# Performance work log

Measured on AMD Instinct MI355X. Metric: run time of the kernel, lower is better.

Reference implementation:

```python
import jax, jax.numpy as jnp
import numpy as np
import math

N = 100000   # nodes
E = 500000   # edges
IN_C = 128
EDGE_D = 64
HEADS = 4
OUT_C = 32
HC = HEADS * OUT_C  # 128


def setup_inputs() -> dict:
    key = jax.random.key(0)
    ks = jax.random.split(key, 12)
    s_in = 1.0 / math.sqrt(IN_C)
    s_e = 1.0 / math.sqrt(EDGE_D)
    return {
        "x": jax.random.normal(ks[0], (N, IN_C), jnp.float32),
        "edge_index": jax.random.randint(ks[1], (2, E), 0, N, dtype=jnp.int32),
        "edge_attr": jax.random.normal(ks[2], (E, EDGE_D), jnp.float32),
        "Wq": jax.random.uniform(ks[3], (HC, IN_C), jnp.float32, -s_in, s_in),
        "bq": jax.random.uniform(ks[4], (HC,), jnp.float32, -s_in, s_in),
        "Wk": jax.random.uniform(ks[5], (HC, IN_C), jnp.float32, -s_in, s_in),
        "bk": jax.random.uniform(ks[6], (HC,), jnp.float32, -s_in, s_in),
        "Wv": jax.random.uniform(ks[7], (HC, IN_C), jnp.float32, -s_in, s_in),
        "bv": jax.random.uniform(ks[8], (HC,), jnp.float32, -s_in, s_in),
        "We": jax.random.uniform(ks[9], (HC, EDGE_D), jnp.float32, -s_e, s_e),
        "Ws": jax.random.uniform(ks[10], (HC, IN_C), jnp.float32, -s_in, s_in),
        "bs": jax.random.uniform(ks[11], (HC,), jnp.float32, -s_in, s_in),
    }


def reference(x, edge_index, edge_attr, Wq, bq, Wk, bk, Wv, bv, We, Ws, bs):
    src = edge_index[0]
    dst = edge_index[1]
    x_i = x[dst]                       # [E, IN_C] target-node feats
    x_j = x[src]                       # [E, IN_C] source-node feats

    e = (edge_attr @ We.T).reshape(E, HEADS, OUT_C)
    q = (x_i @ Wq.T + bq).reshape(E, HEADS, OUT_C)
    k = (x_j @ Wk.T + bk).reshape(E, HEADS, OUT_C) + e

    alpha = jnp.sum(q * k, axis=-1) / jnp.sqrt(jnp.float32(OUT_C))  # [E, H]
    # Faithful to the source: GLOBAL per-column max (not per-segment), then
    # segment-sum of exponentials over destination nodes.
    m = jnp.max(alpha, axis=0)                                      # [H]
    exp_a = jnp.exp(alpha - m)                                      # [E, H]
    denom = jax.ops.segment_sum(exp_a, dst, num_segments=N)         # [N, H]
    alpha = exp_a / (denom[dst] + 1e-16)                            # [E, H]

    v = (x_j @ Wv.T + bv).reshape(E, HEADS, OUT_C) + e
    msg = v * alpha[:, :, None]                                     # [E, H, C]

    out = jax.ops.segment_sum(msg.reshape(E, HC), dst, num_segments=N)  # [N, HC]
    out = out + (x @ Ws.T + bs)
    return out
```

## Files before the change

kernel.cpp:

```cpp
#include <hip/hip_runtime.h>
#include <hip/hip_bf16.h>
#include <math.h>

#define N_NODES 100000
#define N_EDGES 500000
#define M0 8.0f
#define INV_SQRT32 0.17677669529663687f

#define NB_HIST 1954
#define NB_PROJ 1563
#define NB_EE   3907
#define GRID_MEGA (NB_HIST + NB_PROJ + NB_EE)

typedef __attribute__((ext_vector_type(8))) short bf16x8;
typedef __attribute__((ext_vector_type(4))) float f32x4;
typedef __attribute__((ext_vector_type(8))) unsigned short us8;

static __device__ __forceinline__ unsigned short f2bf(float f) {
    __hip_bfloat16 h = __float2bfloat16(f);
    return *(unsigned short*)&h;
}

static __device__ __forceinline__ void split4(float4 v, ushort4& hv, ushort4& lv) {
    const unsigned short h0 = f2bf(v.x), h1 = f2bf(v.y),
                         h2 = f2bf(v.z), h3 = f2bf(v.w);
    hv.x = h0; hv.y = h1; hv.z = h2; hv.w = h3;
    lv.x = f2bf(v.x - __uint_as_float((unsigned)h0 << 16));
    lv.y = f2bf(v.y - __uint_as_float((unsigned)h1 << 16));
    lv.z = f2bf(v.z - __uint_as_float((unsigned)h2 << 16));
    lv.w = f2bf(v.w - __uint_as_float((unsigned)h3 << 16));
}

__global__ __launch_bounds__(256) void prep_kernel(
    const float* __restrict__ Wq, const float* __restrict__ Wk,
    const float* __restrict__ Wv, const float* __restrict__ Ws,
    const float* __restrict__ We,
    unsigned short* __restrict__ WBh, unsigned short* __restrict__ WBl,
    unsigned short* __restrict__ WEh, unsigned short* __restrict__ WEl,
    int* __restrict__ cursor)
{
    const int i = blockIdx.x * 256 + threadIdx.x;
    if (i < N_NODES) cursor[i] = 0;
    if (i < 65536) {
        const int p = i >> 14;
        const float* W = (p == 0) ? Wq : (p == 1) ? Wk : (p == 2) ? Wv : Ws;
        const float v = W[i & 16383];
        const unsigned short h = f2bf(v);
        WBh[i] = h;
        WBl[i] = f2bf(v - __uint_as_float((unsigned)h << 16));
    } else if (i < 73728) {
        const int idx = i - 65536;
        const float v = We[idx];
        const unsigned short h = f2bf(v);
        WEh[idx] = h;
        WEl[idx] = f2bf(v - __uint_as_float((unsigned)h << 16));
    }
}

__global__ __launch_bounds__(256) void mega_kernel(
    const float* __restrict__ x, const int* __restrict__ ei,
    const float* __restrict__ ea,
    const unsigned short* __restrict__ WBh, const unsigned short* __restrict__ WBl,
    const unsigned short* __restrict__ WEh, const unsigned short* __restrict__ WEl,
    const float* __restrict__ bq, const float* __restrict__ bk,
    const float* __restrict__ bv, const float* __restrict__ bs,
    float* __restrict__ Qn, float* __restrict__ Kn, float* __restrict__ Vn,
    float* __restrict__ out, unsigned short* __restrict__ Ee,
    int* __restrict__ cursor)
{
    __shared__ __align__(16) unsigned short sAh[8192];
    __shared__ __align__(16) unsigned short sAl[8192];
    __shared__ __align__(16) unsigned short sWh[8192];
    __shared__ __align__(16) unsigned short sWl[8192];

    const int t = threadIdx.x;
    const int bid = blockIdx.x;

    if (bid < NB_HIST) {
        const int e = bid * 256 + t;
        if (e < N_EDGES) atomicAdd(&cursor[ei[N_EDGES + e]], 1);
        return;
    }

    const int lane = t & 63;
    const int fr = lane & 15;
    const int fq = lane >> 4;

    if (bid < NB_HIST + NB_PROJ) {
        const long r0 = (long)(bid - NB_HIST) * 64;
        const int wid = t >> 6;

        for (int i = t; i < 2048; i += 256) {
            const int r = i >> 5;
            const int k4 = (i & 31) * 4;
            const long row = r0 + r;
            float4 v = (row < N_NODES) ? *(const float4*)&x[row * 128 + k4]
                                       : make_float4(0.f, 0.f, 0.f, 0.f);
            ushort4 hv, lv; split4(v, hv, lv);
            const int di = r * 128 + (k4 ^ ((r & 7) << 3));
            *(ushort4*)&sAh[di] = hv;
            *(ushort4*)&sAl[di] = lv;
        }

        for (int p = 0; p < 4; ++p) {
            const float* bias = (p == 0) ? bq : (p == 1) ? bk : (p == 2) ? bv : bs;
            float* dst        = (p == 0) ? Qn : (p == 1) ? Kn : (p == 2) ? Vn : out;

            f32x4 acc[4][2];
#pragma unroll
            for (int m = 0; m < 4; ++m)
#pragma unroll
                for (int n = 0; n < 2; ++n) acc[m][n] = (f32x4){0.f, 0.f, 0.f, 0.f};

            for (int kc = 0; kc < 2; ++kc) {
                __syncthreads();
                for (int i = t; i < 1024; i += 256) {
                    const int r = i >> 3;
                    const int s = i & 7;
                    const int gi = p * 16384 + r * 128 + kc * 64 + s * 8;
                    const int di = r * 64 + ((s * 8) ^ ((r & 7) << 3));
                    *(us8*)&sWh[di] = *(const us8*)&WBh[gi];
                    *(us8*)&sWl[di] = *(const us8*)&WBl[gi];
                }
                __syncthreads();

#pragma unroll
                for (int ks = 0; ks < 2; ++ks) {
                    const int kx = kc * 64 + ks * 32 + fq * 8;
                    const int kw = ks * 32 + fq * 8;
                    bf16x8 ah[4], al[4], bh[2], bl[2];
#pragma unroll
                    for (int m = 0; m < 4; ++m) {
                        const int r = m * 16 + fr;
                        const int di = r * 128 + (kx ^ ((r & 7) << 3));
                        ah[m] = *(const bf16x8*)&sAh[di];
                        al[m] = *(const bf16x8*)&sAl[di];
                    }
#pragma unroll
                    for (int n = 0; n < 2; ++n) {
                        const int r = wid * 32 + n * 16 + fr;
                        const int di = r * 64 + (kw ^ ((r & 7) << 3));
                        bh[n] = *(const bf16x8*)&sWh[di];
                        bl[n] = *(const bf16x8*)&sWl[di];
                    }
#pragma unroll
                    for (int m = 0; m < 4; ++m)
#pragma unroll
                        for (int n = 0; n < 2; ++n) {
                            acc[m][n] = __builtin_amdgcn_mfma_f32_16x16x32_bf16(
                                ah[m], bh[n], acc[m][n], 0, 0, 0);
                            acc[m][n] = __builtin_amdgcn_mfma_f32_16x16x32_bf16(
                                ah[m], bl[n], acc[m][n], 0, 0, 0);
                            acc[m][n] = __builtin_amdgcn_mfma_f32_16x16x32_bf16(
                                al[m], bh[n], acc[m][n], 0, 0, 0);
                        }
                }
            }

            float bb[2];
#pragma unroll
            for (int n = 0; n < 2; ++n) bb[n] = bias[wid * 32 + n * 16 + fr];
#pragma unroll
            for (int m = 0; m < 4; ++m) {
                const long rowb = r0 + m * 16 + fq * 4;
#pragma unroll
                for (int j = 0; j < 4; ++j) {
                    if (rowb + j < N_NODES) {
#pragma unroll
                        for (int n = 0; n < 2; ++n)
                            dst[(rowb + j) * 128 + wid * 32 + n * 16 + fr] =
                                acc[m][n][j] + bb[n];
                    }
                }
            }
        }
    } else {
        const long e0 = (long)(bid - NB_HIST - NB_PROJ) * 128;
        const int wr = (t >> 6) >> 1;
        const int wc = (t >> 6) & 1;

        for (int i = t; i < 1024; i += 256) {
            const int r = i >> 3;
            const int s = i & 7;
            const int di = r * 64 + ((s * 8) ^ ((r & 7) << 3));
            *(us8*)&sWh[di] = *(const us8*)&WEh[r * 64 + s * 8];
            *(us8*)&sWl[di] = *(const us8*)&WEl[r * 64 + s * 8];
        }
        for (int i = t; i < 2048; i += 256) {
            const int r = i >> 4;
            const int k4 = (i & 15) * 4;
            const long e = e0 + r;
            float4 v = (e < N_EDGES) ? *(const float4*)&ea[e * 64 + k4]
                                     : make_float4(0.f, 0.f, 0.f, 0.f);
            ushort4 hv, lv; split4(v, hv, lv);
            const int di = r * 64 + (k4 ^ ((r & 7) << 3));
            *(ushort4*)&sAh[di] = hv;
            *(ushort4*)&sAl[di] = lv;
        }
        __syncthreads();

        f32x4 acc[4][4];
#pragma unroll
        for (int m = 0; m < 4; ++m)
#pragma unroll
            for (int n = 0; n < 4; ++n) acc[m][n] = (f32x4){0.f, 0.f, 0.f, 0.f};

#pragma unroll
        for (int ks = 0; ks < 2; ++ks) {
            const int kk = ks * 32 + fq * 8;
            bf16x8 ah[4], al[4], bh[4], bl[4];
#pragma unroll
            for (int m = 0; m < 4; ++m) {
                const int r = wr * 64 + m * 16 + fr;
                const int di = r * 64 + (kk ^ ((r & 7) << 3));
                ah[m] = *(const bf16x8*)&sAh[di];
                al[m] = *(const bf16x8*)&sAl[di];
            }
#pragma unroll
            for (int n = 0; n < 4; ++n) {
                const int r = wc * 64 + n * 16 + fr;
                const int di = r * 64 + (kk ^ ((r & 7) << 3));
                bh[n] = *(const bf16x8*)&sWh[di];
                bl[n] = *(const bf16x8*)&sWl[di];
            }
#pragma unroll
            for (int m = 0; m < 4; ++m)
#pragma unroll
                for (int n = 0; n < 4; ++n) {
                    acc[m][n] = __builtin_amdgcn_mfma_f32_16x16x32_bf16(
                        ah[m], bh[n], acc[m][n], 0, 0, 0);
                    acc[m][n] = __builtin_amdgcn_mfma_f32_16x16x32_bf16(
                        ah[m], bl[n], acc[m][n], 0, 0, 0);
                    acc[m][n] = __builtin_amdgcn_mfma_f32_16x16x32_bf16(
                        al[m], bh[n], acc[m][n], 0, 0, 0);
                }
        }

#pragma unroll
        for (int m = 0; m < 4; ++m) {
            const long erow = e0 + wr * 64 + m * 16 + fq * 4;
#pragma unroll
            for (int j = 0; j < 4; ++j) {
                if (erow + j < N_EDGES) {
#pragma unroll
                    for (int n = 0; n < 4; ++n)
                        Ee[(erow + j) * 128 + wc * 64 + n * 16 + fr] =
                            f2bf(acc[m][n][j]);
                }
            }
        }
    }
}

__global__ __launch_bounds__(1024) void csr_scan_kernel(
    int* __restrict__ cursor, int* __restrict__ csr_off)
{
    __shared__ int wsum[16];
    const int t = threadIdx.x;
    const int lane = t & 63;
    const int wid = t >> 6;
    const int n0 = t * 100;
    const bool active = (t < 1000);

    int tsum = 0;
    if (active) {
        for (int q = 0; q < 25; ++q) {
            const int4 d = *(const int4*)&cursor[n0 + q * 4];
            tsum += d.x + d.y + d.z + d.w;
        }
    }
    int inc = tsum;
#pragma unroll
    for (int o = 1; o < 64; o <<= 1) {
        const int v = __shfl_up(inc, o, 64);
        if (lane >= o) inc += v;
    }
    if (lane == 63) wsum[wid] = inc;
    __syncthreads();
    if (t == 0) {
        int run = 0;
#pragma unroll
        for (int w = 0; w < 16; ++w) { const int v = wsum[w]; wsum[w] = run; run += v; }
        csr_off[N_NODES] = run;
    }
    __syncthreads();
    if (active) {
        int run = wsum[wid] + inc - tsum;
        for (int q = 0; q < 25; ++q) {
            const int n = n0 + q * 4;
            const int4 d = *(const int4*)&cursor[n];
            int4 offv;
            offv.x = run; run += d.x;
            offv.y = run; run += d.y;
            offv.z = run; run += d.z;
            offv.w = run; run += d.w;
            *(int4*)&csr_off[n] = offv;
            *(int4*)&cursor[n]  = offv;
        }
    }
}

__global__ __launch_bounds__(256) void csr_fill_kernel(
    const int* __restrict__ ei, int* __restrict__ cursor,
    int* __restrict__ csr_eid, int* __restrict__ csr_src)
{
    const int e = blockIdx.x * 256 + threadIdx.x;
    if (e >= N_EDGES) return;
    const int dst = ei[N_EDGES + e];
    const int pos = atomicAdd(&cursor[dst], 1);
    csr_eid[pos] = e;
    csr_src[pos] = ei[e];
}

__global__ __launch_bounds__(256) void fused_attn_kernel(
    const int* __restrict__ csr_off, const int* __restrict__ csr_eid,
    const int* __restrict__ csr_src, const unsigned short* __restrict__ Ee,
    const float* __restrict__ Qn, const float* __restrict__ Kn,
    const float* __restrict__ Vn, float* __restrict__ out)
{
    const int lane = threadIdx.x & 63;
    const int l2 = lane * 2;
    const long n = (long)blockIdx.x * 4 + (threadIdx.x >> 6);

    const int off0 = csr_off[n];
    const int off1 = csr_off[n + 1];
    const float2 q = *(const float2*)&Qn[n * 128 + l2];

    float dsum = 0.f;
    float2 acc = make_float2(0.f, 0.f);
    for (int base = off0; base < off1; base += 64) {
        const int cnt = min(64, off1 - base);
        int eid = 0, src = 0;
        if (base + lane < off1) {
            eid = csr_eid[base + lane];
            src = csr_src[base + lane];
        }
        for (int j = 0; j < cnt; ++j) {
            const long e = __shfl(eid, j, 64);
            const long s = __shfl(src, j, 64);
            const unsigned u = *(const unsigned*)&Ee[e * 128 + l2];
            const float2 k = *(const float2*)&Kn[s * 128 + l2];
            const float ea0 = __uint_as_float(u << 16);
            const float ea1 = __uint_as_float(u & 0xffff0000u);
            float p = q.x * (k.x + ea0) + q.y * (k.y + ea1);
#pragma unroll
            for (int o = 1; o < 16; o <<= 1) p += __shfl_xor(p, o, 64);
            const float an = __expf(p * INV_SQRT32 - M0);
            dsum += an;
            const float2 v = *(const float2*)&Vn[s * 128 + l2];
            acc.x = fmaf(v.x + ea0, an, acc.x);
            acc.y = fmaf(v.y + ea1, an, acc.y);
        }
    }
    const float rd = 1.f / (dsum + 1e-16f);
    float2 o = *(const float2*)&out[n * 128 + l2];
    o.x = fmaf(acc.x, rd, o.x);
    o.y = fmaf(acc.y, rd, o.y);
    *(float2*)&out[n * 128 + l2] = o;
}

extern "C" void kernel_launch(void* const* d_in, const int* in_sizes, int n_in,
                              void* d_out, int out_size, void* d_ws, size_t ws_size,
                              hipStream_t stream)
{
    const float* x  = (const float*)d_in[0];
    const int*   ei = (const int*)d_in[1];
    const float* ea = (const float*)d_in[2];
    const float* Wq = (const float*)d_in[3];
    const float* bq = (const float*)d_in[4];
    const float* Wk = (const float*)d_in[5];
    const float* bk = (const float*)d_in[6];
    const float* Wv = (const float*)d_in[7];
    const float* bv = (const float*)d_in[8];
    const float* We = (const float*)d_in[9];
    const float* Ws = (const float*)d_in[10];
    const float* bs = (const float*)d_in[11];
    float* out = (float*)d_out;

    float* ws = (float*)d_ws;
    float* Qn = ws;
    float* Kn = ws + 12800000;
    float* Vn = ws + 25600000;
    int* csr_off = (int*)(ws + 38400000);
    int* cursor  = (int*)(ws + 38500004);
    int* csr_eid = (int*)(ws + 38600004);
    int* csr_src = (int*)(ws + 39100004);
    unsigned short* WBh = (unsigned short*)(ws + 40000000);
    unsigned short* WBl = (unsigned short*)(ws + 40050000);
    unsigned short* WEh = (unsigned short*)(ws + 40100000);
    unsigned short* WEl = (unsigned short*)(ws + 40110000);
    unsigned short* Ee = (unsigned short*)((char*)d_ws + 163200032);

    prep_kernel<<<391, 256, 0, stream>>>(Wq, Wk, Wv, Ws, We,
                                         WBh, WBl, WEh, WEl, cursor);

    mega_kernel<<<GRID_MEGA, 256, 0, stream>>>(x, ei, ea,
                                               WBh, WBl, WEh, WEl,
                                               bq, bk, bv, bs,
                                               Qn, Kn, Vn, out, Ee, cursor);

    csr_scan_kernel<<<1, 1024, 0, stream>>>(cursor, csr_off);

    csr_fill_kernel<<<NB_HIST, 256, 0, stream>>>(ei, cursor, csr_eid, csr_src);

    fused_attn_kernel<<<25000, 256, 0, stream>>>(csr_off, csr_eid, csr_src, Ee,
                                                 Qn, Kn, Vn, out);
}
```

Measured before the change: 599.6 us.

## Use 512-thread mega blocks and process four edges per wave in attention

```diff
diff --git a/kernel.cpp b/kernel.cpp
--- a/kernel.cpp
+++ b/kernel.cpp
@@ -7,7 +7,7 @@
 #define M0 8.0f
 #define INV_SQRT32 0.17677669529663687f
 
-#define NB_HIST 1954
+#define NB_HIST 977
 #define NB_PROJ 1563
 #define NB_EE   3907
 #define GRID_MEGA (NB_HIST + NB_PROJ + NB_EE)
@@ -57,7 +57,7 @@
     }
 }
 
-__global__ __launch_bounds__(256) void mega_kernel(
+__global__ __launch_bounds__(512, 4) void mega_kernel(
     const float* __restrict__ x, const int* __restrict__ ei,
     const float* __restrict__ ea,
     const unsigned short* __restrict__ WBh, const unsigned short* __restrict__ WBl,
@@ -77,20 +77,20 @@
     const int bid = blockIdx.x;
 
     if (bid < NB_HIST) {
-        const int e = bid * 256 + t;
+        const int e = bid * 512 + t;
         if (e < N_EDGES) atomicAdd(&cursor[ei[N_EDGES + e]], 1);
         return;
     }
 
     const int lane = t & 63;
+    const int wid = t >> 6;
     const int fr = lane & 15;
     const int fq = lane >> 4;
 
     if (bid < NB_HIST + NB_PROJ) {
         const long r0 = (long)(bid - NB_HIST) * 64;
-        const int wid = t >> 6;
-
-        for (int i = t; i < 2048; i += 256) {
+
+        for (int i = t; i < 2048; i += 512) {
             const int r = i >> 5;
             const int k4 = (i & 31) * 4;
             const long row = r0 + r;
@@ -106,15 +106,13 @@
             const float* bias = (p == 0) ? bq : (p == 1) ? bk : (p == 2) ? bv : bs;
             float* dst        = (p == 0) ? Qn : (p == 1) ? Kn : (p == 2) ? Vn : out;
 
-            f32x4 acc[4][2];
-#pragma unroll
-            for (int m = 0; m < 4; ++m)
-#pragma unroll
-                for (int n = 0; n < 2; ++n) acc[m][n] = (f32x4){0.f, 0.f, 0.f, 0.f};
+            f32x4 acc[4];
+#pragma unroll
+            for (int m = 0; m < 4; ++m) acc[m] = (f32x4){0.f, 0.f, 0.f, 0.f};
 
             for (int kc = 0; kc < 2; ++kc) {
                 __syncthreads();
-                for (int i = t; i < 1024; i += 256) {
+                for (int i = t; i < 1024; i += 512) {
                     const int r = i >> 3;
                     const int s = i & 7;
                     const int gi = p * 16384 + r * 128 + kc * 64 + s * 8;
@@ -128,7 +126,7 @@
                 for (int ks = 0; ks < 2; ++ks) {
                     const int kx = kc * 64 + ks * 32 + fq * 8;
                     const int kw = ks * 32 + fq * 8;
-                    bf16x8 ah[4], al[4], bh[2], bl[2];
+                    bf16x8 ah[4], al[4], bh, bl;
 #pragma unroll
                     for (int m = 0; m < 4; ++m) {
                         const int r = m * 16 + fr;
@@ -136,57 +134,48 @@
                         ah[m] = *(const bf16x8*)&sAh[di];
                         al[m] = *(const bf16x8*)&sAl[di];
                     }
-#pragma unroll
-                    for (int n = 0; n < 2; ++n) {
-                        const int r = wid * 32 + n * 16 + fr;
+                    {
+                        const int r = wid * 16 + fr;
                         const int di = r * 64 + (kw ^ ((r & 7) << 3));
-                        bh[n] = *(const bf16x8*)&sWh[di];
-                        bl[n] = *(const bf16x8*)&sWl[di];
+                        bh = *(const bf16x8*)&sWh[di];
+                        bl = *(const bf16x8*)&sWl[di];
                     }
 #pragma unroll
-                    for (int m = 0; m < 4; ++m)
-#pragma unroll
-                        for (int n = 0; n < 2; ++n) {
-                            acc[m][n] = __builtin_amdgcn_mfma_f32_16x16x32_bf16(
-                                ah[m], bh[n], acc[m][n], 0, 0, 0);
-                            acc[m][n] = __builtin_amdgcn_mfma_f32_16x16x32_bf16(
-                                ah[m], bl[n], acc[m][n], 0, 0, 0);
-                            acc[m][n] = __builtin_amdgcn_mfma_f32_16x16x32_bf16(
-                                al[m], bh[n], acc[m][n], 0, 0, 0);
-                        }
-                }
-            }
-
-            float bb[2];
-#pragma unroll
-            for (int n = 0; n < 2; ++n) bb[n] = bias[wid * 32 + n * 16 + fr];
+                    for (int m = 0; m < 4; ++m) {
+                        acc[m] = __builtin_amdgcn_mfma_f32_16x16x32_bf16(
+                            ah[m], bh, acc[m], 0, 0, 0);
+                        acc[m] = __builtin_amdgcn_mfma_f32_16x16x32_bf16(
+                            ah[m], bl, acc[m], 0, 0, 0);
+                        acc[m] = __builtin_amdgcn_mfma_f32_16x16x32_bf16(
+                            al[m], bh, acc[m], 0, 0, 0);
+                    }
+                }
+            }
+
+            const float bb = bias[wid * 16 + fr];
 #pragma unroll
             for (int m = 0; m < 4; ++m) {
                 const long rowb = r0 + m * 16 + fq * 4;
 #pragma unroll
                 for (int j = 0; j < 4; ++j) {
-                    if (rowb + j < N_NODES) {
-#pragma unroll
-                        for (int n = 0; n < 2; ++n)
-                            dst[(rowb + j) * 128 + wid * 32 + n * 16 + fr] =
-                                acc[m][n][j] + bb[n];
-                    }
+                    if (rowb + j < N_NODES)
+                        dst[(rowb + j) * 128 + wid * 16 + fr] = acc[m][j] + bb;
                 }
             }
         }
     } else {
         const long e0 = (long)(bid - NB_HIST - NB_PROJ) * 128;
-        const int wr = (t >> 6) >> 1;
-        const int wc = (t >> 6) & 1;
-
-        for (int i = t; i < 1024; i += 256) {
+        const int wr = wid >> 2;
+        const int wc = wid & 3;
+
+        for (int i = t; i < 1024; i += 512) {
             const int r = i >> 3;
             const int s = i & 7;
             const int di = r * 64 + ((s * 8) ^ ((r & 7) << 3));
             *(us8*)&sWh[di] = *(const us8*)&WEh[r * 64 + s * 8];
             *(us8*)&sWl[di] = *(const us8*)&WEl[r * 64 + s * 8];
         }
-        for (int i = t; i < 2048; i += 256) {
+        for (int i = t; i < 2048; i += 512) {
             const int r = i >> 4;
             const int k4 = (i & 15) * 4;
             const long e = e0 + r;
@@ -199,16 +188,16 @@
         }
         __syncthreads();
 
-        f32x4 acc[4][4];
+        f32x4 acc[4][2];
 #pragma unroll
         for (int m = 0; m < 4; ++m)
 #pragma unroll
-            for (int n = 0; n < 4; ++n) acc[m][n] = (f32x4){0.f, 0.f, 0.f, 0.f};
+            for (int n = 0; n < 2; ++n) acc[m][n] = (f32x4){0.f, 0.f, 0.f, 0.f};
 
 #pragma unroll
         for (int ks = 0; ks < 2; ++ks) {
             const int kk = ks * 32 + fq * 8;
-            bf16x8 ah[4], al[4], bh[4], bl[4];
+            bf16x8 ah[4], al[4], bh[2], bl[2];
 #pragma unroll
             for (int m = 0; m < 4; ++m) {
                 const int r = wr * 64 + m * 16 + fr;
@@ -217,8 +206,8 @@
                 al[m] = *(const bf16x8*)&sAl[di];
             }
 #pragma unroll
-            for (int n = 0; n < 4; ++n) {
-                const int r = wc * 64 + n * 16 + fr;
+            for (int n = 0; n < 2; ++n) {
+                const int r = wc * 32 + n * 16 + fr;
                 const int di = r * 64 + (kk ^ ((r & 7) << 3));
                 bh[n] = *(const bf16x8*)&sWh[di];
                 bl[n] = *(const bf16x8*)&sWl[di];
@@ -226,7 +215,7 @@
 #pragma unroll
             for (int m = 0; m < 4; ++m)
 #pragma unroll
-                for (int n = 0; n < 4; ++n) {
+                for (int n = 0; n < 2; ++n) {
                     acc[m][n] = __builtin_amdgcn_mfma_f32_16x16x32_bf16(
                         ah[m], bh[n], acc[m][n], 0, 0, 0);
                     acc[m][n] = __builtin_amdgcn_mfma_f32_16x16x32_bf16(
@@ -243,8 +232,8 @@
             for (int j = 0; j < 4; ++j) {
                 if (erow + j < N_EDGES) {
 #pragma unroll
-                    for (int n = 0; n < 4; ++n)
-                        Ee[(erow + j) * 128 + wc * 64 + n * 16 + fr] =
+                    for (int n = 0; n < 2; ++n)
+                        Ee[(erow + j) * 128 + wc * 32 + n * 16 + fr] =
                             f2bf(acc[m][n][j]);
                 }
             }
@@ -319,15 +308,23 @@
     const float* __restrict__ Vn, float* __restrict__ out)
 {
     const int lane = threadIdx.x & 63;
-    const int l2 = lane * 2;
+    const int g = lane >> 4;
+    const int i2 = (lane & 15) * 2;
     const long n = (long)blockIdx.x * 4 + (threadIdx.x >> 6);
 
     const int off0 = csr_off[n];
     const int off1 = csr_off[n + 1];
-    const float2 q = *(const float2*)&Qn[n * 128 + l2];
-
-    float dsum = 0.f;
-    float2 acc = make_float2(0.f, 0.f);
+
+    float2 q[4];
+#pragma unroll
+    for (int h = 0; h < 4; ++h)
+        q[h] = *(const float2*)&Qn[n * 128 + h * 32 + i2];
+
+    float dsum[4] = {0.f, 0.f, 0.f, 0.f};
+    float2 acc[4];
+#pragma unroll
+    for (int h = 0; h < 4; ++h) acc[h] = make_float2(0.f, 0.f);
+
     for (int base = off0; base < off1; base += 64) {
         const int cnt = min(64, off1 - base);
         int eid = 0, src = 0;
@@ -335,28 +332,63 @@
             eid = csr_eid[base + lane];
             src = csr_src[base + lane];
         }
-        for (int j = 0; j < cnt; ++j) {
+        for (int c0 = 0; c0 < cnt; c0 += 4) {
+            const int j = c0 + g;
+            const bool valid = (j < cnt);
             const long e = __shfl(eid, j, 64);
             const long s = __shfl(src, j, 64);
-            const unsigned u = *(const unsigned*)&Ee[e * 128 + l2];
-            const float2 k = *(const float2*)&Kn[s * 128 + l2];
-            const float ea0 = __uint_as_float(u << 16);
-            const float ea1 = __uint_as_float(u & 0xffff0000u);
-            float p = q.x * (k.x + ea0) + q.y * (k.y + ea1);
-#pragma unroll
-            for (int o = 1; o < 16; o <<= 1) p += __shfl_xor(p, o, 64);
-            const float an = __expf(p * INV_SQRT32 - M0);
-            dsum += an;
-            const float2 v = *(const float2*)&Vn[s * 128 + l2];
-            acc.x = fmaf(v.x + ea0, an, acc.x);
-            acc.y = fmaf(v.y + ea1, an, acc.y);
-        }
-    }
-    const float rd = 1.f / (dsum + 1e-16f);
-    float2 o = *(const float2*)&out[n * 128 + l2];
-    o.x = fmaf(acc.x, rd, o.x);
-    o.y = fmaf(acc.y, rd, o.y);
-    *(float2*)&out[n * 128 + l2] = o;
+
+            float ph[4];
+            float ea0[4], ea1[4];
+            float2 vv[4];
+            if (valid) {
+#pragma unroll
+                for (int h = 0; h < 4; ++h) {
+                    const int ch = h * 32 + i2;
+                    const unsigned u = *(const unsigned*)&Ee[e * 128 + ch];
+                    ea0[h] = __uint_as_float(u << 16);
+                    ea1[h] = __uint_as_float(u & 0xffff0000u);
+                    const float2 k = *(const float2*)&Kn[s * 128 + ch];
+                    vv[h] = *(const float2*)&Vn[s * 128 + ch];
+                    ph[h] = q[h].x * (k.x + ea0[h]) + q[h].y * (k.y + ea1[h]);
+                }
+            } else {
+#pragma unroll
+                for (int h = 0; h < 4; ++h) ph[h] = 0.f;
+            }
+#pragma unroll
+            for (int h = 0; h < 4; ++h) {
+#pragma unroll
+                for (int o = 1; o < 16; o <<= 1)
+                    ph[h] += __shfl_xor(ph[h], o, 64);
+            }
+            if (valid) {
+#pragma unroll
+                for (int h = 0; h < 4; ++h) {
+                    const float an = __expf(ph[h] * INV_SQRT32 - M0);
+                    dsum[h] += an;
+                    acc[h].x = fmaf(vv[h].x + ea0[h], an, acc[h].x);
+                    acc[h].y = fmaf(vv[h].y + ea1[h], an, acc[h].y);
+                }
+            }
+        }
+    }
+
+#pragma unroll
+    for (int h = 0; h < 4; ++h) {
+#pragma unroll
+        for (int o = 16; o < 64; o <<= 1) {
+            dsum[h] += __shfl_xor(dsum[h], o, 64);
+            acc[h].x += __shfl_xor(acc[h].x, o, 64);
+            acc[h].y += __shfl_xor(acc[h].y, o, 64);
+        }
+    }
+
+    const float rd = 1.f / (dsum[g] + 1e-16f);
+    float2 o = *(const float2*)&out[n * 128 + g * 32 + i2];
+    o.x = fmaf(acc[g].x, rd, o.x);
+    o.y = fmaf(acc[g].y, rd, o.y);
+    *(float2*)&out[n * 128 + g * 32 + i2] = o;
 }
 
 extern "C" void kernel_launch(void* const* d_in, const int* in_sizes, int n_in,
@@ -394,14 +426,15 @@
     prep_kernel<<<391, 256, 0, stream>>>(Wq, Wk, Wv, Ws, We,
                                          WBh, WBl, WEh, WEl, cursor);
 
-    mega_kernel<<<GRID_MEGA, 256, 0, stream>>>(x, ei, ea,
+    mega_kernel<<<GRID_MEGA, 512, 0, stream>>>(x, ei, ea,
                                                WBh, WBl, WEh, WEl,
                                                bq, bk, bv, bs,
                                                Qn, Kn, Vn, out, Ee, cursor);
 
     csr_scan_kernel<<<1, 1024, 0, stream>>>(cursor, csr_off);
 
-    csr_fill_kernel<<<NB_HIST, 256, 0, stream>>>(ei, cursor, csr_eid, csr_src);
+    csr_fill_kernel<<<(N_EDGES + 255) / 256, 256, 0, stream>>>(ei, cursor,
+                                                               csr_eid, csr_src);
 
     fused_attn_kernel<<<25000, 256, 0, stream>>>(csr_off, csr_eid, csr_src, Ee,
                                                  Qn, Kn, Vn, out);
```

New measurement: 575.9 us. 1.04x faster.
